# Performance work log

Hardware: AMD Instinct MI355X
Metric: run time of the kernel (lower is better)

## Reference

```python
import jax, jax.numpy as jnp
import numpy as np

N_BITS = 8  # abits = wbits = 8 (symmetric signed per-tensor quant)
QN = -2 ** (N_BITS - 1)
QP = 2 ** (N_BITS - 1) - 1


def _round_pass(v):
    # straight-through round: forward round, backward identity
    return v + jax.lax.stop_gradient(jnp.round(v) - v)


def _quantize(t):
    # per-tensor symmetric quantization; scale detached like torch .detach()
    scale = jax.lax.stop_gradient(jnp.max(jnp.abs(t))) / QP
    q = _round_pass(jnp.clip(t / scale, QN, QP))
    return q, scale


def _quantized_linear(x3, s_x, w, b):
    # x3: [B, S, Din]; w: [Dout, Din]; b: [Dout]; s_x: scalar dequant scale
    B, S, Din = x3.shape
    x2 = x3.reshape(-1, Din) * s_x              # dequantize incoming activations
    qw, sw = _quantize(w)
    qx, sx = _quantize(x2)
    out = jnp.matmul(qx, qw.T)                  # int-valued float GEMM
    out = out + b[None, :]                      # bias added before rescale (as in source)
    return (out * (sw * sx)).reshape(B, S, -1)


def setup_inputs() -> dict:
    key = jax.random.key(0)
    k1, k2, k3, k4, k5 = jax.random.split(key, 5)
    B, S, D, H = 128, 197, 384, 1536
    x = jax.random.normal(k1, (B, S, D), dtype=jnp.float32)
    act_scaling_factor = jnp.ones((1,), dtype=jnp.float32)
    w1 = jax.random.normal(k2, (H, D), dtype=jnp.float32) * (1.0 / np.sqrt(D))
    b1 = jax.random.normal(k3, (H,), dtype=jnp.float32) * 0.02
    w2 = jax.random.normal(k4, (D, H), dtype=jnp.float32) * (1.0 / np.sqrt(H))
    b2 = jax.random.normal(k5, (D,), dtype=jnp.float32) * 0.02
    return {"x": x, "act_scaling_factor": act_scaling_factor,
            "w1": w1, "b1": b1, "w2": w2, "b2": b2}


def reference(x, act_scaling_factor, w1, b1, w2, b2):
    s_x = act_scaling_factor.reshape(())
    h = _quantized_linear(x, s_x, w1, b1)       # fc1
    h = jax.nn.gelu(h, approximate=False)       # torch nn.GELU (erf)
    qh, s_h = _quantize(h)                      # qact1: requantize activations
    out = _quantized_linear(qh, s_h, w2, b2)    # fc2
    return out
```

## Files before the change

kernel.cpp:

```cpp
#include <hip/hip_runtime.h>
#include <hip/hip_bf16.h>
#include <stdint.h>

typedef int v4i __attribute__((ext_vector_type(4)));

#define GPTR(p) ((const __attribute__((address_space(1))) void*)(p))
#define LPTR(p) ((__attribute__((address_space(3))) void*)(p))

__device__ __forceinline__ float wave_max(float m) {
#pragma unroll
  for (int off = 32; off > 0; off >>= 1)
    m = fmaxf(m, __shfl_xor(m, off, 64));
  return m;
}

__device__ __forceinline__ float gelu_tanh(float x) {
  const float x2 = x * x;
  const float u = x * fmaf(0.044715f, x2, 1.0f);
  const float e = exp2f(-2.3022082f * u);
  return x * __builtin_amdgcn_rcpf(1.0f + e);
}

__global__ void absmax3_kernel(const float* __restrict__ x, int nx4,
                               const float* __restrict__ smul,
                               const float* __restrict__ w1, int nw14,
                               const float* __restrict__ w2, int nw24,
                               unsigned* __restrict__ scal) {
  __shared__ float red[4];
  const int bid = blockIdx.x;
  const float4* s4;
  int n4, b0, nb;
  float s = 1.0f;
  unsigned* dst;
  if (bid < 512)      { s4 = (const float4*)x;  n4 = nx4;  s = smul[0]; dst = scal;     b0 = bid;       nb = 512; }
  else if (bid < 640) { s4 = (const float4*)w1; n4 = nw14;              dst = scal + 1; b0 = bid - 512; nb = 128; }
  else                { s4 = (const float4*)w2; n4 = nw24;              dst = scal + 2; b0 = bid - 640; nb = 128; }
  float m = 0.0f;
  const int stride = nb * blockDim.x;
  for (int i = b0 * blockDim.x + threadIdx.x; i < n4; i += stride) {
    float4 v = s4[i];
    m = fmaxf(m, fabsf(v.x * s));
    m = fmaxf(m, fabsf(v.y * s));
    m = fmaxf(m, fabsf(v.z * s));
    m = fmaxf(m, fabsf(v.w * s));
  }
  m = wave_max(m);
  if ((threadIdx.x & 63) == 0) red[threadIdx.x >> 6] = m;
  __syncthreads();
  if (threadIdx.x == 0)
    atomicMax(dst, __float_as_uint(fmaxf(fmaxf(red[0], red[1]), fmaxf(red[2], red[3]))));
}

__global__ void quantize3_kernel(const float* __restrict__ x, int nx4,
                                 const float* __restrict__ smul,
                                 const float* __restrict__ w1, int nw14,
                                 const float* __restrict__ w2, int nw24,
                                 const unsigned* __restrict__ scal,
                                 int8_t* __restrict__ qx,
                                 int8_t* __restrict__ qw1,
                                 int8_t* __restrict__ qw2) {
  const int bid = blockIdx.x;
  const float4* s4;
  char4* d4;
  int n4, b0, nb;
  float s = 1.0f, mx;
  if (bid < 2048)      { s4 = (const float4*)x;  d4 = (char4*)qx;  n4 = nx4;  s = smul[0]; mx = __uint_as_float(scal[0]); b0 = bid;        nb = 2048; }
  else if (bid < 2176) { s4 = (const float4*)w1; d4 = (char4*)qw1; n4 = nw14;              mx = __uint_as_float(scal[1]); b0 = bid - 2048; nb = 128; }
  else                 { s4 = (const float4*)w2; d4 = (char4*)qw2; n4 = nw24;              mx = __uint_as_float(scal[2]); b0 = bid - 2176; nb = 128; }
  const float scale = mx / 127.0f;
  const int stride = nb * blockDim.x;
  for (int i = b0 * blockDim.x + threadIdx.x; i < n4; i += stride) {
    float4 v = s4[i];
    char4 qq;
    qq.x = (signed char)(int)rintf(fminf(fmaxf((v.x * s) / scale, -128.0f), 127.0f));
    qq.y = (signed char)(int)rintf(fminf(fmaxf((v.y * s) / scale, -128.0f), 127.0f));
    qq.z = (signed char)(int)rintf(fminf(fmaxf((v.z * s) / scale, -128.0f), 127.0f));
    qq.w = (signed char)(int)rintf(fminf(fmaxf((v.w * s) / scale, -128.0f), 127.0f));
    d4[i] = qq;
  }
}

__global__ void reduce_scale_kernel(const float* __restrict__ partial, int n,
                                    unsigned* __restrict__ scal) {
  __shared__ float red[4];
  float m = -3.4e38f;
  for (int i = threadIdx.x; i < n; i += blockDim.x) m = fmaxf(m, partial[i]);
  m = wave_max(m);
  if ((threadIdx.x & 63) == 0) red[threadIdx.x >> 6] = m;
  __syncthreads();
  if (threadIdx.x == 0) {
    m = fmaxf(fmaxf(red[0], red[1]), fmaxf(red[2], red[3]));
    const float sx = __uint_as_float(scal[0]) / 127.0f;
    const float sw = __uint_as_float(scal[1]) / 127.0f;
    const float max_f = m * (sw * sx);
    scal[3] = __float_as_uint(fmaxf(gelu_tanh(max_f), 0.1699702f));
  }
}

template <int EPI>
__device__ __forceinline__
void gemm_body(const int8_t* __restrict__ A, const int8_t* __restrict__ B,
               const float* __restrict__ bias, const unsigned* __restrict__ scal,
               float* __restrict__ partial, int8_t* __restrict__ out_i8,
               float* __restrict__ out_f32, int N, int K, int GN) {
  __shared__ __align__(16) int8_t lA[2][128 * 64];
  __shared__ __align__(16) int8_t lB[2][128 * 64];
  __shared__ float red8[8];

  const int nwg = gridDim.x;
  const int q = nwg >> 3, rr = nwg & 7;
  const int xcd = blockIdx.x & 7, sub = blockIdx.x >> 3;
  const int wg = (xcd < rr ? xcd * (q + 1) : rr * (q + 1) + (xcd - rr) * q) + sub;
  const int bx = wg % GN;
  const int by = wg / GN;
  const int tid0 = by * GN + bx;

  const int t = threadIdx.x;
  const int lane = t & 63;
  const int wave = t >> 6;
  const int wr = wave >> 1;
  const int wc = wave & 1;
  const size_t m0 = (size_t)by * 128;
  const int n0 = bx * 128;

  const int8_t* Ab = A + m0 * (size_t)K;
  const int8_t* Bb = B + (size_t)n0 * (size_t)K;

  v4i acc[2][4] = {};
  const int KT = K >> 6;

  const int row0 = t >> 2;
  const int ss = (t & 3) ^ ((row0 >> 1) & 3);
  const int ubase = __builtin_amdgcn_readfirstlane(wave * 1024);
  const size_t srcA0 = (size_t)row0 * K + (size_t)(ss * 16);

  auto stage = [&](int buf, int kt) {
    const int8_t* ga = Ab + kt * 64;
    const int8_t* gb = Bb + kt * 64;
    __builtin_amdgcn_global_load_lds(GPTR(ga + srcA0), LPTR(&lA[buf][ubase]), 16, 0, 0);
    __builtin_amdgcn_global_load_lds(GPTR(gb + srcA0), LPTR(&lB[buf][ubase]), 16, 0, 0);
  };

  const int r15 = lane & 15;
  const int q4 = lane >> 4;

  auto compute = [&](int buf) {
    v4i af[2], bf[4];
#pragma unroll
    for (int fr = 0; fr < 2; ++fr) {
      const int row = wr * 32 + fr * 16 + r15;
      const int slot = q4 ^ ((row >> 1) & 3);
      af[fr] = *(const v4i*)(&lA[buf][row * 64 + slot * 16]);
    }
#pragma unroll
    for (int fc = 0; fc < 4; ++fc) {
      const int row = wc * 64 + fc * 16 + r15;
      const int slot = q4 ^ ((row >> 1) & 3);
      bf[fc] = *(const v4i*)(&lB[buf][row * 64 + slot * 16]);
    }
#pragma unroll
    for (int fr = 0; fr < 2; ++fr)
#pragma unroll
      for (int fc = 0; fc < 4; ++fc)
        acc[fr][fc] = __builtin_amdgcn_mfma_i32_16x16x64_i8(af[fr], bf[fc], acc[fr][fc], 0, 0, 0);
  };

  stage(0, 0);
  __syncthreads();
  int cur = 0;
  for (int kt = 1; kt < KT; ++kt) {
    stage(cur ^ 1, kt);
    compute(cur);
    __syncthreads();
    cur ^= 1;
  }
  compute(cur);

  const int rb = q4 * 4;

  if constexpr (EPI == 0) {
    float lm = -3.4e38f;
#pragma unroll
    for (int fc = 0; fc < 4; ++fc) {
      int im = acc[0][fc][0];
#pragma unroll
      for (int fr = 0; fr < 2; ++fr)
#pragma unroll
        for (int r = 0; r < 4; ++r) im = max(im, acc[fr][fc][r]);
      lm = fmaxf(lm, (float)im + bias[n0 + wc * 64 + fc * 16 + r15]);
    }
    lm = wave_max(lm);
    if (lane == 0) red8[wave] = lm;
    __syncthreads();
    if (t == 0) {
      float bm = red8[0];
#pragma unroll
      for (int w = 1; w < 8; ++w) bm = fmaxf(bm, red8[w]);
      partial[tid0] = bm;
    }
  } else if constexpr (EPI == 1) {
    const float sx = __uint_as_float(scal[0]) / 127.0f;
    const float sw = __uint_as_float(scal[1]) / 127.0f;
    const float s1 = sw * sx;
    const float sh = __uint_as_float(scal[3]) / 127.0f;
    const float inv_sh = __builtin_amdgcn_rcpf(sh);
    __syncthreads();
    int8_t* qt = (int8_t*)lA;
#pragma unroll
    for (int fc = 0; fc < 4; ++fc) {
      const int col = wc * 64 + fc * 16 + r15;
      const float bvs = bias[n0 + col] * s1;
#pragma unroll
      for (int fr = 0; fr < 2; ++fr) {
        const int rowb = wr * 32 + fr * 16 + rb;
#pragma unroll
        for (int r = 0; r < 4; ++r) {
          const float f = fmaf((float)acc[fr][fc][r], s1, bvs);
          const float g = gelu_tanh(f);
          const float qv = rintf(fminf(fmaxf(g * inv_sh, -128.0f), 127.0f));
          qt[(rowb + r) * 128 + (col ^ (q4 << 4))] = (int8_t)(int)qv;
        }
      }
    }
    __syncthreads();
#pragma unroll
    for (int v = 0; v < 2; ++v) {
      const int idx = v * 512 + t;
      const int row = idx >> 3;
      const int colb = (idx & 7) * 16;
      const int swz = ((row >> 2) & 3) << 4;
      *(v4i*)(out_i8 + (m0 + row) * (size_t)N + n0 + colb) =
          *(const v4i*)(qt + row * 128 + (colb ^ swz));
    }
  } else {
    const float sw2 = __uint_as_float(scal[2]) / 127.0f;
    const float sh = __uint_as_float(scal[3]) / 127.0f;
    const float s2 = sw2 * ((127.0f * sh) / 127.0f);
#pragma unroll
    for (int fc = 0; fc < 4; ++fc) {
      const int n = n0 + wc * 64 + fc * 16 + r15;
      const float bvs = bias[n] * s2;
#pragma unroll
      for (int fr = 0; fr < 2; ++fr)
#pragma unroll
        for (int r = 0; r < 4; ++r) {
          const size_t m = m0 + (size_t)(wr * 32 + fr * 16 + rb + r);
          out_f32[m * (size_t)N + n] = fmaf((float)acc[fr][fc][r], s2, bvs);
        }
    }
  }
}

__global__ __launch_bounds__(512, 4)
void gemm1_absmax_kernel(const int8_t* A, const int8_t* B, const float* bias,
                         const unsigned* scal, float* partial, int N, int K, int GN) {
  gemm_body<0>(A, B, bias, scal, partial, nullptr, nullptr, N, K, GN);
}

__global__ __launch_bounds__(512, 4)
void gemm1_quant_kernel(const int8_t* A, const int8_t* B, const float* bias,
                        const unsigned* scal, int8_t* out_i8, int N, int K, int GN) {
  gemm_body<1>(A, B, bias, scal, nullptr, out_i8, nullptr, N, K, GN);
}

__global__ __launch_bounds__(512, 4)
void gemm2_out_kernel(const int8_t* A, const int8_t* B, const float* bias,
                      const unsigned* scal, float* out_f32, int N, int K, int GN) {
  gemm_body<2>(A, B, bias, scal, nullptr, nullptr, out_f32, N, K, GN);
}

extern "C" void kernel_launch(void* const* d_in, const int* in_sizes, int n_in,
                              void* d_out, int out_size, void* d_ws, size_t ws_size,
                              hipStream_t stream) {
  const float* x   = (const float*)d_in[0];
  const float* sxp = (const float*)d_in[1];
  const float* w1  = (const float*)d_in[2];
  const float* b1  = (const float*)d_in[3];
  const float* w2  = (const float*)d_in[4];
  const float* b2  = (const float*)d_in[5];

  const int H = in_sizes[3];
  const int D = in_sizes[5];
  const int M = in_sizes[0] / D;
  const int GM = M / 128;
  const int GN1 = H / 128;
  const int GN2 = D / 128;

  uint8_t* ws = (uint8_t*)d_ws;
  unsigned* scal = (unsigned*)ws;
  size_t off = 256;
  float* partial = (float*)(ws + off); off += 16384;
  int8_t* qx  = (int8_t*)(ws + off); off += (size_t)M * D;
  int8_t* qw1 = (int8_t*)(ws + off); off += (size_t)H * D;
  int8_t* qw2 = (int8_t*)(ws + off); off += (size_t)D * H;
  int8_t* qh  = (int8_t*)(ws + off); off += (size_t)M * H;
  (void)ws_size; (void)n_in; (void)out_size;

  hipMemsetAsync(scal, 0, 16, stream);

  absmax3_kernel<<<dim3(768), dim3(256), 0, stream>>>(
      x, M * D / 4, sxp, w1, H * D / 4, w2, D * H / 4, scal);

  quantize3_kernel<<<dim3(2304), dim3(256), 0, stream>>>(
      x, M * D / 4, sxp, w1, H * D / 4, w2, D * H / 4, scal, qx, qw1, qw2);

  dim3 blk(512);
  dim3 g1(GN1 * GM);
  gemm1_absmax_kernel<<<g1, blk, 0, stream>>>(qx, qw1, b1, scal, partial, H, D, GN1);
  reduce_scale_kernel<<<1, 256, 0, stream>>>(partial, GM * GN1, scal);
  gemm1_quant_kernel<<<g1, blk, 0, stream>>>(qx, qw1, b1, scal, qh, H, D, GN1);

  dim3 g2(GN2 * GM);
  gemm2_out_kernel<<<g2, blk, 0, stream>>>(qh, qw2, b2, scal, (float*)d_out, D, H, GN2);
}
```

Baseline: 132.0 us.

## Specialize fc1 GEMM with 64-row tiles and whole-K LDS preload

Splits fc1 into a dedicated kernel that uses 64x128 tiles with 256 threads and loads the entire K=384 slab of A and B into LDS up front via direct global-to-LDS loads. The per-K-step double-buffered pipeline and its barriers are removed, and the grid doubles to spread the two fc1 passes across more workgroups. The cost is more LDS per block (about 72KB), which limits occupancy, and no overlap between loads and MFMA within a block. The partial-max buffer is enlarged to hold the larger grid.

Measured after the change: 137.2 us. 1.04x slower.

```diff
diff --git a/kernel.cpp b/kernel.cpp
--- a/kernel.cpp
+++ b/kernel.cpp
@@ -98,14 +98,14 @@
 }
 
 template <int EPI>
-__device__ __forceinline__
-void gemm_body(const int8_t* __restrict__ A, const int8_t* __restrict__ B,
-               const float* __restrict__ bias, const unsigned* __restrict__ scal,
-               float* __restrict__ partial, int8_t* __restrict__ out_i8,
-               float* __restrict__ out_f32, int N, int K, int GN) {
-  __shared__ __align__(16) int8_t lA[2][128 * 64];
-  __shared__ __align__(16) int8_t lB[2][128 * 64];
-  __shared__ float red8[8];
+__global__ __launch_bounds__(256, 2)
+void fc1_kernel(const int8_t* __restrict__ A, const int8_t* __restrict__ B,
+                const float* __restrict__ bias, const unsigned* __restrict__ scal,
+                float* __restrict__ partial, int8_t* __restrict__ qh,
+                int N, int K, int GN) {
+  __shared__ __align__(16) int8_t lA[6][64 * 64];
+  __shared__ __align__(16) int8_t lB[6][128 * 64];
+  __shared__ float red4[4];
 
   const int nwg = gridDim.x;
   const int q = nwg >> 3, rr = nwg & 7;
@@ -114,6 +114,126 @@
   const int bx = wg % GN;
   const int by = wg / GN;
   const int tid0 = by * GN + bx;
+
+  const int t = threadIdx.x;
+  const int lane = t & 63;
+  const int wave = t >> 6;
+  const int wr = wave >> 1;
+  const int wc = wave & 1;
+  const int r15 = lane & 15;
+  const int q4 = lane >> 4;
+  const size_t m0 = (size_t)by * 64;
+  const int n0 = bx * 128;
+
+  const int8_t* Ab = A + m0 * (size_t)K;
+  const int8_t* Bb = B + (size_t)n0 * (size_t)K;
+
+  const int row0 = t >> 2;
+  const int ss = (t & 3) ^ ((row0 >> 1) & 3);
+  const int ubase = __builtin_amdgcn_readfirstlane((t & 192) * 16);
+  const size_t srcA  = (size_t)row0 * K + (size_t)(ss * 16);
+  const size_t srcB1 = (size_t)(row0 + 64) * K + (size_t)(ss * 16);
+
+#pragma unroll
+  for (int c = 0; c < 6; ++c) {
+    __builtin_amdgcn_global_load_lds(GPTR(Ab + c * 64 + srcA),  LPTR(&lA[c][ubase]), 16, 0, 0);
+    __builtin_amdgcn_global_load_lds(GPTR(Bb + c * 64 + srcA),  LPTR(&lB[c][ubase]), 16, 0, 0);
+    __builtin_amdgcn_global_load_lds(GPTR(Bb + c * 64 + srcB1), LPTR(&lB[c][4096 + ubase]), 16, 0, 0);
+  }
+  asm volatile("s_waitcnt vmcnt(0)" ::: "memory");
+  __syncthreads();
+
+  v4i acc[2][4] = {};
+#pragma unroll
+  for (int kt = 0; kt < 6; ++kt) {
+    v4i af[2], bf[4];
+#pragma unroll
+    for (int fr = 0; fr < 2; ++fr) {
+      const int row = wr * 32 + fr * 16 + r15;
+      const int slot = q4 ^ ((row >> 1) & 3);
+      af[fr] = *(const v4i*)(&lA[kt][row * 64 + slot * 16]);
+    }
+#pragma unroll
+    for (int fc = 0; fc < 4; ++fc) {
+      const int row = wc * 64 + fc * 16 + r15;
+      const int slot = q4 ^ ((row >> 1) & 3);
+      bf[fc] = *(const v4i*)(&lB[kt][row * 64 + slot * 16]);
+    }
+#pragma unroll
+    for (int fr = 0; fr < 2; ++fr)
+#pragma unroll
+      for (int fc = 0; fc < 4; ++fc)
+        acc[fr][fc] = __builtin_amdgcn_mfma_i32_16x16x64_i8(af[fr], bf[fc], acc[fr][fc], 0, 0, 0);
+  }
+
+  const int rb = q4 * 4;
+
+  if constexpr (EPI == 0) {
+    float lm = -3.4e38f;
+#pragma unroll
+    for (int fc = 0; fc < 4; ++fc) {
+      int im = acc[0][fc][0];
+#pragma unroll
+      for (int fr = 0; fr < 2; ++fr)
+#pragma unroll
+        for (int r = 0; r < 4; ++r) im = max(im, acc[fr][fc][r]);
+      lm = fmaxf(lm, (float)im + bias[n0 + wc * 64 + fc * 16 + r15]);
+    }
+    lm = wave_max(lm);
+    if (lane == 0) red4[wave] = lm;
+    __syncthreads();
+    if (t == 0)
+      partial[tid0] = fmaxf(fmaxf(red4[0], red4[1]), fmaxf(red4[2], red4[3]));
+  } else {
+    const float sx = __uint_as_float(scal[0]) / 127.0f;
+    const float sw = __uint_as_float(scal[1]) / 127.0f;
+    const float s1 = sw * sx;
+    const float sh = __uint_as_float(scal[3]) / 127.0f;
+    const float inv_sh = __builtin_amdgcn_rcpf(sh);
+    __syncthreads();
+    int8_t* qt = (int8_t*)lA;
+#pragma unroll
+    for (int fc = 0; fc < 4; ++fc) {
+      const int col = wc * 64 + fc * 16 + r15;
+      const float bvs = bias[n0 + col] * s1;
+#pragma unroll
+      for (int fr = 0; fr < 2; ++fr) {
+        const int rowb = wr * 32 + fr * 16 + rb;
+#pragma unroll
+        for (int r = 0; r < 4; ++r) {
+          const float f = fmaf((float)acc[fr][fc][r], s1, bvs);
+          const float g = gelu_tanh(f);
+          const float qv = rintf(fminf(fmaxf(g * inv_sh, -128.0f), 127.0f));
+          qt[(rowb + r) * 128 + (col ^ (q4 << 4))] = (int8_t)(int)qv;
+        }
+      }
+    }
+    __syncthreads();
+#pragma unroll
+    for (int v = 0; v < 2; ++v) {
+      const int idx = v * 256 + t;
+      const int row = idx >> 3;
+      const int colb = (idx & 7) * 16;
+      const int swz = ((row >> 2) & 3) << 4;
+      *(v4i*)(qh + (m0 + row) * (size_t)N + n0 + colb) =
+          *(const v4i*)(qt + row * 128 + (colb ^ swz));
+    }
+  }
+}
+
+__global__ __launch_bounds__(512, 4)
+void gemm2_out_kernel(const int8_t* __restrict__ A, const int8_t* __restrict__ B,
+                      const float* __restrict__ bias, const unsigned* __restrict__ scal,
+                      float* __restrict__ out_f32, int N, int K, int GN) {
+  __shared__ __align__(16) int8_t lA[2][128 * 64];
+  __shared__ __align__(16) int8_t lB[2][128 * 64];
+
+  const int nwg = gridDim.x;
+  const int q = nwg >> 3, rr = nwg & 7;
+  const int xcd = blockIdx.x & 7, sub = blockIdx.x >> 3;
+  const int wg = (xcd < rr ? xcd * (q + 1) : rr * (q + 1) + (xcd - rr) * q) + sub;
+  const int bx = wg % GN;
+  const int by = wg / GN;
 
   const int t = threadIdx.x;
   const int lane = t & 63;
@@ -177,96 +297,21 @@
   compute(cur);
 
   const int rb = q4 * 4;
-
-  if constexpr (EPI == 0) {
-    float lm = -3.4e38f;
-#pragma unroll
-    for (int fc = 0; fc < 4; ++fc) {
-      int im = acc[0][fc][0];
-#pragma unroll
-      for (int fr = 0; fr < 2; ++fr)
-#pragma unroll
-        for (int r = 0; r < 4; ++r) im = max(im, acc[fr][fc][r]);
-      lm = fmaxf(lm, (float)im + bias[n0 + wc * 64 + fc * 16 + r15]);
-    }
-    lm = wave_max(lm);
-    if (lane == 0) red8[wave] = lm;
-    __syncthreads();
-    if (t == 0) {
-      float bm = red8[0];
-#pragma unroll
-      for (int w = 1; w < 8; ++w) bm = fmaxf(bm, red8[w]);
-      partial[tid0] = bm;
-    }
-  } else if constexpr (EPI == 1) {
-    const float sx = __uint_as_float(scal[0]) / 127.0f;
-    const float sw = __uint_as_float(scal[1]) / 127.0f;
-    const float s1 = sw * sx;
-    const float sh = __uint_as_float(scal[3]) / 127.0f;
-    const float inv_sh = __builtin_amdgcn_rcpf(sh);
-    __syncthreads();
-    int8_t* qt = (int8_t*)lA;
-#pragma unroll
-    for (int fc = 0; fc < 4; ++fc) {
-      const int col = wc * 64 + fc * 16 + r15;
-      const float bvs = bias[n0 + col] * s1;
-#pragma unroll
-      for (int fr = 0; fr < 2; ++fr) {
-        const int rowb = wr * 32 + fr * 16 + rb;
-#pragma unroll
-        for (int r = 0; r < 4; ++r) {
-          const float f = fmaf((float)acc[fr][fc][r], s1, bvs);
-          const float g = gelu_tanh(f);
-          const float qv = rintf(fminf(fmaxf(g * inv_sh, -128.0f), 127.0f));
-          qt[(rowb + r) * 128 + (col ^ (q4 << 4))] = (int8_t)(int)qv;
-        }
+  const float sw2 = __uint_as_float(scal[2]) / 127.0f;
+  const float sh = __uint_as_float(scal[3]) / 127.0f;
+  const float s2 = sw2 * ((127.0f * sh) / 127.0f);
+#pragma unroll
+  for (int fc = 0; fc < 4; ++fc) {
+    const int n = n0 + wc * 64 + fc * 16 + r15;
+    const float bvs = bias[n] * s2;
+#pragma unroll
+    for (int fr = 0; fr < 2; ++fr)
+#pragma unroll
+      for (int r = 0; r < 4; ++r) {
+        const size_t m = m0 + (size_t)(wr * 32 + fr * 16 + rb + r);
+        out_f32[m * (size_t)N + n] = fmaf((float)acc[fr][fc][r], s2, bvs);
       }
-    }
-    __syncthreads();
-#pragma unroll
-    for (int v = 0; v < 2; ++v) {
-      const int idx = v * 512 + t;
-      const int row = idx >> 3;
-      const int colb = (idx & 7) * 16;
-      const int swz = ((row >> 2) & 3) << 4;
-      *(v4i*)(out_i8 + (m0 + row) * (size_t)N + n0 + colb) =
-          *(const v4i*)(qt + row * 128 + (colb ^ swz));
-    }
-  } else {
-    const float sw2 = __uint_as_float(scal[2]) / 127.0f;
-    const float sh = __uint_as_float(scal[3]) / 127.0f;
-    const float s2 = sw2 * ((127.0f * sh) / 127.0f);
-#pragma unroll
-    for (int fc = 0; fc < 4; ++fc) {
-      const int n = n0 + wc * 64 + fc * 16 + r15;
-      const float bvs = bias[n] * s2;
-#pragma unroll
-      for (int fr = 0; fr < 2; ++fr)
-#pragma unroll
-        for (int r = 0; r < 4; ++r) {
-          const size_t m = m0 + (size_t)(wr * 32 + fr * 16 + rb + r);
-          out_f32[m * (size_t)N + n] = fmaf((float)acc[fr][fc][r], s2, bvs);
-        }
-    }
-  }
-}
-
-__global__ __launch_bounds__(512, 4)
-void gemm1_absmax_kernel(const int8_t* A, const int8_t* B, const float* bias,
-                         const unsigned* scal, float* partial, int N, int K, int GN) {
-  gemm_body<0>(A, B, bias, scal, partial, nullptr, nullptr, N, K, GN);
-}
-
-__global__ __launch_bounds__(512, 4)
-void gemm1_quant_kernel(const int8_t* A, const int8_t* B, const float* bias,
-                        const unsigned* scal, int8_t* out_i8, int N, int K, int GN) {
-  gemm_body<1>(A, B, bias, scal, nullptr, out_i8, nullptr, N, K, GN);
-}
-
-__global__ __launch_bounds__(512, 4)
-void gemm2_out_kernel(const int8_t* A, const int8_t* B, const float* bias,
-                      const unsigned* scal, float* out_f32, int N, int K, int GN) {
-  gemm_body<2>(A, B, bias, scal, nullptr, nullptr, out_f32, N, K, GN);
+  }
 }
 
 extern "C" void kernel_launch(void* const* d_in, const int* in_sizes, int n_in,
@@ -282,14 +327,15 @@
   const int H = in_sizes[3];
   const int D = in_sizes[5];
   const int M = in_sizes[0] / D;
-  const int GM = M / 128;
+  const int GM1 = M / 64;
+  const int GM2 = M / 128;
   const int GN1 = H / 128;
   const int GN2 = D / 128;
 
   uint8_t* ws = (uint8_t*)d_ws;
   unsigned* scal = (unsigned*)ws;
   size_t off = 256;
-  float* partial = (float*)(ws + off); off += 16384;
+  float* partial = (float*)(ws + off); off += 32768;
   int8_t* qx  = (int8_t*)(ws + off); off += (size_t)M * D;
   int8_t* qw1 = (int8_t*)(ws + off); off += (size_t)H * D;
   int8_t* qw2 = (int8_t*)(ws + off); off += (size_t)D * H;
@@ -304,12 +350,11 @@
   quantize3_kernel<<<dim3(2304), dim3(256), 0, stream>>>(
       x, M * D / 4, sxp, w1, H * D / 4, w2, D * H / 4, scal, qx, qw1, qw2);
 
-  dim3 blk(512);
-  dim3 g1(GN1 * GM);
-  gemm1_absmax_kernel<<<g1, blk, 0, stream>>>(qx, qw1, b1, scal, partial, H, D, GN1);
-  reduce_scale_kernel<<<1, 256, 0, stream>>>(partial, GM * GN1, scal);
-  gemm1_quant_kernel<<<g1, blk, 0, stream>>>(qx, qw1, b1, scal, qh, H, D, GN1);
-
-  dim3 g2(GN2 * GM);
-  gemm2_out_kernel<<<g2, blk, 0, stream>>>(qh, qw2, b2, scal, (float*)d_out, D, H, GN2);
-}
+  dim3 g1(GN1 * GM1);
+  fc1_kernel<0><<<g1, dim3(256), 0, stream>>>(qx, qw1, b1, scal, partial, nullptr, H, D, GN1);
+  reduce_scale_kernel<<<1, 256, 0, stream>>>(partial, GM1 * GN1, scal);
+  fc1_kernel<1><<<g1, dim3(256), 0, stream>>>(qx, qw1, b1, scal, nullptr, qh, H, D, GN1);
+
+  dim3 g2(GN2 * GM2);
+  gemm2_out_kernel<<<g2, dim3(512), 0, stream>>>(qh, qw2, b2, scal, (float*)d_out, D, H, GN2);
+}
```
